# Performance work log

Hardware: AMD Instinct MI355X
Metric: run time of the kernel (lower is better)

## Reference

```python
import jax, jax.numpy as jnp
import numpy as np

N, DEG, F, H, O, B = 100000, 16, 128, 128, 128, 8192


def setup_inputs() -> dict:
    key = jax.random.key(0)
    k1, k2, k3, k4, k5 = jax.random.split(key, 5)
    features = jax.random.normal(k1, (N, F), dtype=jnp.float32)
    w1 = jax.random.normal(k2, (2 * F, H), dtype=jnp.float32)
    w2 = jax.random.normal(k3, (2 * H, O), dtype=jnp.float32)
    neighbor_idx = jax.random.randint(k4, (N, DEG), 0, N, dtype=jnp.int32)
    nodes = jax.random.randint(k5, (B,), 0, N, dtype=jnp.int32)
    return {"features": features, "w1": w1, "w2": w2,
            "neighbor_idx": neighbor_idx, "nodes": nodes}


def reference(features, w1, w2, neighbor_idx, nodes):
    # Layer 1 (computed for all nodes, vectorized): mean-aggregate neighbor
    # raw features, concat with self features, project with w1.
    neigh_feat = features[neighbor_idx]                 # [N, DEG, F] gather
    agg1 = neigh_feat.mean(axis=1)                      # [N, F]
    h1 = jnp.concatenate([features, agg1], axis=-1) @ w1  # [N, H]

    # Layer 2 (batch nodes): mean-aggregate neighbor layer-1 embeddings,
    # concat with self layer-1 embedding, project with w2.
    h1_self = h1[nodes]                                 # [B, H]
    h1_neigh = h1[neighbor_idx[nodes]].mean(axis=1)     # [B, H]
    out = jnp.concatenate([h1_self, h1_neigh], axis=-1) @ w2  # [B, O]
    return out
```

## Files before the change

### kernel.cpp

```cpp
#include <hip/hip_runtime.h>


#define N_NODES 100000
#define DEG     16
#define FDIM    128
#define HDIM    128
#define B_NODES 8192

typedef __attribute__((ext_vector_type(8))) short bf16x8;
typedef __attribute__((ext_vector_type(8))) unsigned short u16x8;
typedef __attribute__((ext_vector_type(4))) float f32x4;
typedef __attribute__((ext_vector_type(2))) float f32x2;

static __device__ __forceinline__ unsigned short f2bf(float f) {
    union { float f; unsigned u; } v; v.f = f;
    unsigned r = v.u + 0x7fff + ((v.u >> 16) & 1);
    return (unsigned short)(r >> 16);
}
static __device__ __forceinline__ float bf2f(unsigned short b) {
    union { unsigned u; float f; } v; v.u = ((unsigned)b) << 16;
    return v.f;
}

__global__ __launch_bounds__(256)
void prep(const float* __restrict__ feat, const float* __restrict__ w1,
          const float* __restrict__ w2, unsigned short* __restrict__ fb,
          unsigned char* __restrict__ f8s,
          unsigned short* __restrict__ w1T, unsigned short* __restrict__ w2T) {
    if (blockIdx.x < 6250) {
        long e = ((long)blockIdx.x * 256 + threadIdx.x) * 8;
        float4 v0 = *(const float4*)(feat + e);
        float4 v1 = *(const float4*)(feat + e + 4);
        u16x8 ob;
        ob[0] = f2bf(v0.x); ob[1] = f2bf(v0.y); ob[2] = f2bf(v0.z); ob[3] = f2bf(v0.w);
        ob[4] = f2bf(v1.x); ob[5] = f2bf(v1.y); ob[6] = f2bf(v1.z); ob[7] = f2bf(v1.w);
        *(u16x8*)(fb + e) = ob;
        int p0 = 0, p1 = 0;
        p0 = __builtin_amdgcn_cvt_pk_fp8_f32(v0.x, v0.y, p0, false);
        p0 = __builtin_amdgcn_cvt_pk_fp8_f32(v0.z, v0.w, p0, true);
        p1 = __builtin_amdgcn_cvt_pk_fp8_f32(v1.x, v1.y, p1, false);
        p1 = __builtin_amdgcn_cvt_pk_fp8_f32(v1.z, v1.w, p1, true);
        int node = (int)(e >> 7), col = (int)(e & 127);
        int slice = col >> 5;
        unsigned char* dst = f8s + (long)slice * (N_NODES * 32) + (long)node * 32 + (col & 31);
        uint2 o8; o8.x = (unsigned)p0; o8.y = (unsigned)p1;
        *(uint2*)dst = o8;
    } else {
        int bid = blockIdx.x - 6250;
        const float* w = (bid < 8) ? w1 : w2;
        unsigned short* wT = (bid < 8) ? w1T : w2T;
        int kb = (bid & 7) * 32;
        int n = threadIdx.x & 127, dk = threadIdx.x >> 7;
#pragma unroll
        for (int i = 0; i < 16; ++i) {
            int k = kb + dk * 16 + i;
            wT[n * 256 + k] = f2bf(w[k * 128 + n]);
        }
    }
}

__global__ __launch_bounds__(256)
void k1_agg(const unsigned char* __restrict__ f8s, const int* __restrict__ nbr,
            unsigned short* __restrict__ agg) {
    const int t = threadIdx.x, b = blockIdx.x;
    const int s = (b & 7) >> 1;
    const int chunk = ((b >> 3) << 1) + (b & 1);
    const int node = chunk * 64 + (t >> 2);
    if (node >= N_NODES) return;
    const int q = t & 3;
    const unsigned char* base = f8s + (long)s * (N_NODES * 32) + q * 8;
    const int* idx = nbr + node * DEG;
    int4 i0 = *(const int4*)(idx);
    int4 i1 = *(const int4*)(idx + 4);
    int4 i2 = *(const int4*)(idx + 8);
    int4 i3 = *(const int4*)(idx + 12);
    int id[16] = {i0.x, i0.y, i0.z, i0.w, i1.x, i1.y, i1.z, i1.w,
                  i2.x, i2.y, i2.z, i2.w, i3.x, i3.y, i3.z, i3.w};
    uint2 v[16];
#pragma unroll
    for (int d = 0; d < DEG; ++d)
        v[d] = *(const uint2*)(base + (long)id[d] * 32);
    float sm[8] = {0.f, 0.f, 0.f, 0.f, 0.f, 0.f, 0.f, 0.f};
#pragma unroll
    for (int d = 0; d < DEG; ++d) {
        f32x2 a0 = __builtin_amdgcn_cvt_pk_f32_fp8((int)v[d].x, false);
        f32x2 a1 = __builtin_amdgcn_cvt_pk_f32_fp8((int)v[d].x, true);
        f32x2 a2 = __builtin_amdgcn_cvt_pk_f32_fp8((int)v[d].y, false);
        f32x2 a3 = __builtin_amdgcn_cvt_pk_f32_fp8((int)v[d].y, true);
        sm[0] += a0[0]; sm[1] += a0[1]; sm[2] += a1[0]; sm[3] += a1[1];
        sm[4] += a2[0]; sm[5] += a2[1]; sm[6] += a3[0]; sm[7] += a3[1];
    }
    u16x8 o;
#pragma unroll
    for (int j = 0; j < 8; ++j) o[j] = f2bf(sm[j] * 0.0625f);
    *(u16x8*)(agg + (long)node * 128 + s * 32 + q * 8) = o;
}

#define STAGE(KC, BUF)                                                                        \
    do {                                                                                      \
        const unsigned short* s0_ = ((KC) < 4) ? (fb + (KC) * 32) : (agg + ((KC) - 4) * 32);  \
        _Pragma("unroll")                                                                     \
        for (int j_ = 0; j_ < 2; ++j_) {                                                      \
            long grow_ = row0 + (t >> 2) + j_ * 64;                                           \
            const unsigned short* ga_ = s0_ + grow_ * 128 + (t & 3) * 8;                      \
            __builtin_amdgcn_global_load_lds(                                                 \
                (const __attribute__((address_space(1))) unsigned int*)ga_,                   \
                (__attribute__((address_space(3))) unsigned int*)                             \
                    (&AsS[(BUF) * 4096 + wave * 512 + j_ * 2048 + lane * 8]), 16, 0, 0);      \
            const unsigned short* gw_ = w1T + ((t >> 2) + j_ * 64) * 256 + (KC) * 32 + (t & 3) * 8; \
            __builtin_amdgcn_global_load_lds(                                                 \
                (const __attribute__((address_space(1))) unsigned int*)gw_,                   \
                (__attribute__((address_space(3))) unsigned int*)                             \
                    (&WsS[(BUF) * 4096 + wave * 512 + j_ * 2048 + lane * 8]), 16, 0, 0);      \
        }                                                                                     \
    } while (0)

__global__ __launch_bounds__(256, 2)
void g1(const unsigned short* __restrict__ fb, const unsigned short* __restrict__ agg,
        const unsigned short* __restrict__ w1T, unsigned short* __restrict__ h1) {
    __shared__ unsigned short AsS[2 * 4096];
    __shared__ unsigned short WsS[2 * 4096];
    const int t = threadIdx.x, wave = t >> 6, lane = t & 63;
    const int m16 = lane & 15, quad = lane >> 4;
    const long row0 = (long)blockIdx.x * 128;

    f32x4 acc[2][8] = {};
    STAGE(0, 0);
#pragma unroll
    for (int kc = 0; kc < 8; ++kc) {
        __syncthreads();
        if (kc < 7) {
            switch (kc + 1) {
                case 1: STAGE(1, 1); break;
                case 2: STAGE(2, 0); break;
                case 3: STAGE(3, 1); break;
                case 4: STAGE(4, 0); break;
                case 5: STAGE(5, 1); break;
                case 6: STAGE(6, 0); break;
                case 7: STAGE(7, 1); break;
            }
        }
        const unsigned short* Ab = &AsS[(kc & 1) * 4096];
        const unsigned short* Wb = &WsS[(kc & 1) * 4096];
        bf16x8 a0 = *(const bf16x8*)(Ab + (wave * 32 + m16) * 32 + quad * 8);
        bf16x8 a1 = *(const bf16x8*)(Ab + (wave * 32 + 16 + m16) * 32 + quad * 8);
#pragma unroll
        for (int nt = 0; nt < 8; ++nt) {
            bf16x8 bv = *(const bf16x8*)(Wb + (nt * 16 + m16) * 32 + quad * 8);
            acc[0][nt] = __builtin_amdgcn_mfma_f32_16x16x32_bf16(a0, bv, acc[0][nt], 0, 0, 0);
            acc[1][nt] = __builtin_amdgcn_mfma_f32_16x16x32_bf16(a1, bv, acc[1][nt], 0, 0, 0);
        }
    }

#pragma unroll
    for (int mt = 0; mt < 2; ++mt)
#pragma unroll
        for (int reg = 0; reg < 4; ++reg) {
            long grow = row0 + wave * 32 + mt * 16 + quad * 4 + reg;
            if (grow >= N_NODES) continue;
#pragma unroll
            for (int nt = 0; nt < 8; ++nt)
                h1[grow * HDIM + nt * 16 + m16] = f2bf(acc[mt][nt][reg]);
        }
}

__global__ __launch_bounds__(256)
void g2_fused(const unsigned short* __restrict__ h1, const unsigned short* __restrict__ w2T,
              const int* __restrict__ nbr, const int* __restrict__ nodes,
              float* __restrict__ out) {
    __shared__ unsigned short X2[64][264];
    const int t = threadIdx.x, wave = t >> 6, lane = t & 63;
    const int m16 = lane & 15, quad = lane >> 4;
    const int b0 = blockIdx.x * 64;
    const int colb = m16 * 8;

    for (int g = 0; g < 4; ++g) {
        int Ln = wave * 16 + g * 4 + quad;
        int node = nodes[b0 + Ln];
        *(u16x8*)(&X2[Ln][colb]) = *(const u16x8*)(h1 + node * HDIM + colb);
        const int* idx = nbr + node * DEG;
        float s[8] = {0.f, 0.f, 0.f, 0.f, 0.f, 0.f, 0.f, 0.f};
#pragma unroll
        for (int d = 0; d < DEG; ++d) {
            int nb = idx[d];
            u16x8 v = *(const u16x8*)(h1 + nb * HDIM + colb);
#pragma unroll
            for (int j = 0; j < 8; ++j) s[j] += bf2f(v[j]);
        }
        u16x8 o;
#pragma unroll
        for (int j = 0; j < 8; ++j) o[j] = f2bf(s[j] * 0.0625f);
        *(u16x8*)(&X2[Ln][128 + colb]) = o;
    }
    __syncthreads();

    f32x4 acc[8] = {};
#pragma unroll
    for (int kc = 0; kc < 8; ++kc) {
        bf16x8 a = *(const bf16x8*)(&X2[wave * 16 + m16][kc * 32 + quad * 8]);
#pragma unroll
        for (int nt = 0; nt < 8; ++nt) {
            bf16x8 b = *(const bf16x8*)(w2T + (nt * 16 + m16) * 256 + kc * 32 + quad * 8);
            acc[nt] = __builtin_amdgcn_mfma_f32_16x16x32_bf16(a, b, acc[nt], 0, 0, 0);
        }
    }

#pragma unroll
    for (int nt = 0; nt < 8; ++nt)
#pragma unroll
        for (int reg = 0; reg < 4; ++reg) {
            int row = b0 + wave * 16 + quad * 4 + reg;
            out[row * 128 + nt * 16 + m16] = acc[nt][reg];
        }
}

extern "C" void kernel_launch(void* const* d_in, const int* in_sizes, int n_in,
                              void* d_out, int out_size, void* d_ws, size_t ws_size,
                              hipStream_t stream) {
    const float* feat  = (const float*)d_in[0];
    const float* w1    = (const float*)d_in[1];
    const float* w2    = (const float*)d_in[2];
    const int*   nbr   = (const int*)d_in[3];
    const int*   nodes = (const int*)d_in[4];
    float* out = (float*)d_out;

    char* ws = (char*)d_ws;
    unsigned short* fb  = (unsigned short*)ws;
    unsigned char*  f8s = (unsigned char*)(ws + 25600000);
    unsigned short* agg = (unsigned short*)(ws + 38400000);
    unsigned short* h1  = (unsigned short*)(ws + 64000000);
    unsigned short* w1T = (unsigned short*)(ws + 89600000);
    unsigned short* w2T = (unsigned short*)(ws + 89665536);

    prep<<<6266, 256, 0, stream>>>(feat, w1, w2, fb, f8s, w1T, w2T);
    k1_agg<<<6256, 256, 0, stream>>>(f8s, nbr, agg);
    g1<<<(N_NODES + 127) / 128, 256, 0, stream>>>(fb, agg, w1T, h1);
    g2_fused<<<B_NODES / 64, 256, 0, stream>>>(h1, w2T, nbr, nodes, out);
}
```

Baseline: 173.1 us.

## Gather full fp8 feature rows via direct global-to-LDS loads in aggregation

Stores the fp8 feature copy in plain row-major layout instead of four 32-column slices. The aggregation kernel now has 8 threads each fetch a 16-byte piece of a 128-byte neighbor row and load it asynchronously into shared memory with global_load_lds. The intent is to cut gather transactions by fetching whole contiguous rows with wider accesses, and to halve the block count. In exchange it uses 64KB of LDS per block, which may limit occupancy and latency hiding, and adds a block-wide barrier.

```diff
diff --git a/kernel.cpp b/kernel.cpp
--- a/kernel.cpp
+++ b/kernel.cpp
@@ -25,7 +25,7 @@
 __global__ __launch_bounds__(256)
 void prep(const float* __restrict__ feat, const float* __restrict__ w1,
           const float* __restrict__ w2, unsigned short* __restrict__ fb,
-          unsigned char* __restrict__ f8s,
+          unsigned char* __restrict__ f8,
           unsigned short* __restrict__ w1T, unsigned short* __restrict__ w2T) {
     if (blockIdx.x < 6250) {
         long e = ((long)blockIdx.x * 256 + threadIdx.x) * 8;
@@ -40,11 +40,8 @@
         p0 = __builtin_amdgcn_cvt_pk_fp8_f32(v0.z, v0.w, p0, true);
         p1 = __builtin_amdgcn_cvt_pk_fp8_f32(v1.x, v1.y, p1, false);
         p1 = __builtin_amdgcn_cvt_pk_fp8_f32(v1.z, v1.w, p1, true);
-        int node = (int)(e >> 7), col = (int)(e & 127);
-        int slice = col >> 5;
-        unsigned char* dst = f8s + (long)slice * (N_NODES * 32) + (long)node * 32 + (col & 31);
         uint2 o8; o8.x = (unsigned)p0; o8.y = (unsigned)p1;
-        *(uint2*)dst = o8;
+        *(uint2*)(f8 + e) = o8;
     } else {
         int bid = blockIdx.x - 6250;
         const float* w = (bid < 8) ? w1 : w2;
@@ -60,40 +57,54 @@
 }
 
 __global__ __launch_bounds__(256)
-void k1_agg(const unsigned char* __restrict__ f8s, const int* __restrict__ nbr,
+void k1_agg(const unsigned char* __restrict__ f8, const int* __restrict__ nbr,
             unsigned short* __restrict__ agg) {
-    const int t = threadIdx.x, b = blockIdx.x;
-    const int s = (b & 7) >> 1;
-    const int chunk = ((b >> 3) << 1) + (b & 1);
-    const int node = chunk * 64 + (t >> 2);
-    if (node >= N_NODES) return;
-    const int q = t & 3;
-    const unsigned char* base = f8s + (long)s * (N_NODES * 32) + q * 8;
+    __shared__ unsigned char L[4][16][1024];
+    const int t = threadIdx.x, wave = t >> 6, lane = t & 63;
+    const int node = blockIdx.x * 32 + (t >> 3);
+    const int sub = t & 7;
     const int* idx = nbr + node * DEG;
     int4 i0 = *(const int4*)(idx);
     int4 i1 = *(const int4*)(idx + 4);
     int4 i2 = *(const int4*)(idx + 8);
     int4 i3 = *(const int4*)(idx + 12);
-    int id[16] = {i0.x, i0.y, i0.z, i0.w, i1.x, i1.y, i1.z, i1.w,
-                  i2.x, i2.y, i2.z, i2.w, i3.x, i3.y, i3.z, i3.w};
-    uint2 v[16];
-#pragma unroll
-    for (int d = 0; d < DEG; ++d)
-        v[d] = *(const uint2*)(base + (long)id[d] * 32);
-    float sm[8] = {0.f, 0.f, 0.f, 0.f, 0.f, 0.f, 0.f, 0.f};
+    const int id[16] = {i0.x, i0.y, i0.z, i0.w, i1.x, i1.y, i1.z, i1.w,
+                        i2.x, i2.y, i2.z, i2.w, i3.x, i3.y, i3.z, i3.w};
 #pragma unroll
     for (int d = 0; d < DEG; ++d) {
-        f32x2 a0 = __builtin_amdgcn_cvt_pk_f32_fp8((int)v[d].x, false);
-        f32x2 a1 = __builtin_amdgcn_cvt_pk_f32_fp8((int)v[d].x, true);
-        f32x2 a2 = __builtin_amdgcn_cvt_pk_f32_fp8((int)v[d].y, false);
-        f32x2 a3 = __builtin_amdgcn_cvt_pk_f32_fp8((int)v[d].y, true);
-        sm[0] += a0[0]; sm[1] += a0[1]; sm[2] += a1[0]; sm[3] += a1[1];
-        sm[4] += a2[0]; sm[5] += a2[1]; sm[6] += a3[0]; sm[7] += a3[1];
-    }
-    u16x8 o;
-#pragma unroll
-    for (int j = 0; j < 8; ++j) o[j] = f2bf(sm[j] * 0.0625f);
-    *(u16x8*)(agg + (long)node * 128 + s * 32 + q * 8) = o;
+        const unsigned char* src = f8 + (long)id[d] * 128 + sub * 16;
+        __builtin_amdgcn_global_load_lds(
+            (const __attribute__((address_space(1))) unsigned int*)src,
+            (__attribute__((address_space(3))) unsigned int*)(&L[wave][d][lane * 16]),
+            16, 0, 0);
+    }
+    __syncthreads();
+
+    float s[16];
+#pragma unroll
+    for (int j = 0; j < 16; ++j) s[j] = 0.f;
+#pragma unroll
+    for (int d = 0; d < DEG; ++d) {
+        uint4 v = *(const uint4*)(&L[wave][d][lane * 16]);
+        f32x2 c;
+        c = __builtin_amdgcn_cvt_pk_f32_fp8((int)v.x, false); s[0]  += c[0]; s[1]  += c[1];
+        c = __builtin_amdgcn_cvt_pk_f32_fp8((int)v.x, true);  s[2]  += c[0]; s[3]  += c[1];
+        c = __builtin_amdgcn_cvt_pk_f32_fp8((int)v.y, false); s[4]  += c[0]; s[5]  += c[1];
+        c = __builtin_amdgcn_cvt_pk_f32_fp8((int)v.y, true);  s[6]  += c[0]; s[7]  += c[1];
+        c = __builtin_amdgcn_cvt_pk_f32_fp8((int)v.z, false); s[8]  += c[0]; s[9]  += c[1];
+        c = __builtin_amdgcn_cvt_pk_f32_fp8((int)v.z, true);  s[10] += c[0]; s[11] += c[1];
+        c = __builtin_amdgcn_cvt_pk_f32_fp8((int)v.w, false); s[12] += c[0]; s[13] += c[1];
+        c = __builtin_amdgcn_cvt_pk_f32_fp8((int)v.w, true);  s[14] += c[0]; s[15] += c[1];
+    }
+    u16x8 o0, o1;
+#pragma unroll
+    for (int j = 0; j < 8; ++j) {
+        o0[j] = f2bf(s[j] * 0.0625f);
+        o1[j] = f2bf(s[8 + j] * 0.0625f);
+    }
+    unsigned short* dst = agg + (long)node * 128 + sub * 16;
+    *(u16x8*)dst = o0;
+    *(u16x8*)(dst + 8) = o1;
 }
 
 #define STAGE(KC, BUF)                                                                        \
@@ -226,14 +237,14 @@
 
     char* ws = (char*)d_ws;
     unsigned short* fb  = (unsigned short*)ws;
-    unsigned char*  f8s = (unsigned char*)(ws + 25600000);
+    unsigned char*  f8  = (unsigned char*)(ws + 25600000);
     unsigned short* agg = (unsigned short*)(ws + 38400000);
     unsigned short* h1  = (unsigned short*)(ws + 64000000);
     unsigned short* w1T = (unsigned short*)(ws + 89600000);
     unsigned short* w2T = (unsigned short*)(ws + 89665536);
 
-    prep<<<6266, 256, 0, stream>>>(feat, w1, w2, fb, f8s, w1T, w2T);
-    k1_agg<<<6256, 256, 0, stream>>>(f8s, nbr, agg);
+    prep<<<6266, 256, 0, stream>>>(feat, w1, w2, fb, f8, w1T, w2T);
+    k1_agg<<<3125, 256, 0, stream>>>(f8, nbr, agg);
     g1<<<(N_NODES + 127) / 128, 256, 0, stream>>>(fb, agg, w1T, h1);
     g2_fused<<<B_NODES / 64, 256, 0, stream>>>(h1, w2T, nbr, nodes, out);
 }
```

Result: faster. 165.9 us (-4.2%).
